# Kernel tuning notes

Hardware: AMD Instinct MI355X
Metric: run time of the kernel (lower is better)

Reference implementation:

```python
import jax, jax.numpy as jnp
import numpy as np
import math

# ---- static config (matches init_kwargs) ----
MUL = 16                       # multiplicity of 0e and 1o irreps in/out
IN_DIM = 4 * MUL               # 16x0e + 16x1o -> 16 + 48 = 64 channels
DIAMETER = 7.0
RADIUS = DIAMETER / 2.0
NRB = 8                        # num_radial_basis
STEPS = (1.0, 1.0, 1.0)
N_PATHS = 5                    # 0x0->0, 1x1->0, 0x1->1, 1x0->1, 1x1->1
WEIGHT_NUMEL = N_PATHS * MUL * MUL  # 1280


def _lattice():
    axes = []
    for st in STEPS:
        s = math.floor(RADIUS / st)
        axes.append(np.arange(-s, s + 1.0) * st)
    return np.stack(np.meshgrid(*axes, indexing='ij'), axis=-1).astype(np.float32)  # [kx,ky,kz,3]


def _radial_emb(r):
    # e3nn soft_one_hot_linspace, basis='smooth_finite', cutoff=True
    values = np.linspace(0.0, RADIUS, NRB + 2)[1:-1].astype(np.float32)
    step = values[1] - values[0]
    diff = (r[..., None] - values) / step
    def u(t):  # soft unit step: exp(-1/t) for t>0 else 0
        return np.where(t > 0.0, np.exp(-1.0 / np.where(t > 0.0, t, 1.0)), 0.0)
    return (1.14136 * math.e ** 2 * u(diff + 1.0) * u(1.0 - diff)).astype(np.float32)


def _spherical_harmonics(lat):
    # normalize=True, normalization='component': Y0 = 1, Y1 = sqrt(3) * unit_vec
    n = np.linalg.norm(lat, axis=-1, keepdims=True)
    unit = np.where(n > 0, lat / np.where(n > 0, n, 1.0), 0.0)
    return np.ones(lat.shape[:-1], np.float32), (math.sqrt(3.0) * unit).astype(np.float32)


_LAT = _lattice()
_EMB = jnp.asarray(_radial_emb(np.linalg.norm(_LAT, axis=-1)))  # [kx,ky,kz,NRB]
_sh0_np, _sh1_np = _spherical_harmonics(_LAT)
_SH0, _SH1 = jnp.asarray(_sh0_np), jnp.asarray(_sh1_np)
_eps_np = np.zeros((3, 3, 3), np.float32)
for _i, _j, _k in [(0, 1, 2), (1, 2, 0), (2, 0, 1)]:
    _eps_np[_i, _j, _k] = 1.0
    _eps_np[_i, _k, _j] = -1.0
_EPS = jnp.asarray(_eps_np)


def _build_kernel(tp_weight):
    """Radial-basis matmul + CG tensor-product -> conv kernel [out,in,kx,ky,kz]."""
    kx, ky, kz = _LAT.shape[:3]
    nk = kx * ky * kz
    w = jnp.einsum('xyzb,bn->xyzn', _EMB, tp_weight) / nk
    w = w.reshape(kx, ky, kz, N_PATHS, MUL, MUL)
    w1, w2, w3, w4, w5 = [w[..., p, :, :] for p in range(N_PATHS)]
    # e3nn path weights ('component' norm, 'element' path norm): sqrt(dim_out / fan_in)
    a0 = math.sqrt(1.0 / (2 * MUL))  # -> 0e: paths 1,2 each mul1*mul2 = MUL
    a1 = math.sqrt(3.0 / (3 * MUL))  # -> 1o: paths 3,4,5
    c1 = a0                          # w3j(0,0,0) = 1
    c2 = a0 / math.sqrt(3.0)         # w3j(1,1,0) = delta/sqrt(3)
    c3 = a1 / math.sqrt(3.0)         # w3j(0,1,1) = delta/sqrt(3)
    c4 = a1 / math.sqrt(3.0)         # w3j(1,0,1) = delta/sqrt(3)
    c5 = a1 / math.sqrt(6.0)         # w3j(1,1,1) = eps/sqrt(6)
    Kss = c1 * _SH0[..., None, None] * w1                                  # [k,u,o]
    Kvs = c2 * jnp.einsum('xyzi,xyzuo->xyzuio', _SH1, w2)                  # [k,u,3,o]
    Ksv = c3 * jnp.einsum('xyzk,xyzuo->xyzuok', _SH1, w3)                  # [k,u,o,3]
    eye3 = jnp.eye(3, dtype=w.dtype)
    Kvv = (c4 * jnp.einsum('xyz,ik,xyzuo->xyzuiok', _SH0, eye3, w4)
           + c5 * jnp.einsum('ijk,xyzj,xyzuo->xyzuiok', _EPS, _SH1, w5))   # [k,u,3,o,3]
    top = jnp.concatenate([Kss, Ksv.reshape(kx, ky, kz, MUL, 3 * MUL)], axis=-1)
    bot = jnp.concatenate([Kvs.reshape(kx, ky, kz, 3 * MUL, MUL),
                           Kvv.reshape(kx, ky, kz, 3 * MUL, 3 * MUL)], axis=-1)
    K = jnp.concatenate([top, bot], axis=-2)                               # [kx,ky,kz,in,out]
    return jnp.transpose(K, (4, 3, 0, 1, 2))                               # oixyz


def setup_inputs() -> dict:
    key = jax.random.key(0)
    k1, k2, k3, k4 = jax.random.split(key, 4)
    x = jax.random.normal(k1, (2, IN_DIM, 40, 40, 40), jnp.float32)
    sc_w0 = jax.random.normal(k2, (MUL, MUL), jnp.float32)
    sc_w1 = jax.random.normal(k3, (MUL, MUL), jnp.float32)
    tp_weight = jax.random.normal(k4, (NRB, WEIGHT_NUMEL), jnp.float32)
    return {"x": x, "sc_w0": sc_w0, "sc_w1": sc_w1, "tp_weight": tp_weight}


def reference(x, sc_w0, sc_w1, tp_weight):
    B = x.shape[0]
    sp = x.shape[2:]
    inv = 1.0 / math.sqrt(MUL)  # e3nn Linear fan-in normalization
    x0 = x[:, :MUL]                                  # [B,MUL,D,H,W]
    x1 = x[:, MUL:].reshape(B, MUL, 3, *sp)          # [B,MUL,3,D,H,W]
    sc0 = jnp.einsum('uo,budhw->bodhw', sc_w0, x0) * inv
    sc1 = jnp.einsum('uo,buidhw->boidhw', sc_w1, x1) * inv
    sc = jnp.concatenate([sc0, sc1.reshape(B, 3 * MUL, *sp)], axis=1)
    K = _build_kernel(tp_weight)
    pad = [(s // 2, s // 2) for s in K.shape[2:]]
    conv = jax.lax.conv_general_dilated(
        x, K, window_strides=(1, 1, 1), padding=pad,
        dimension_numbers=('NCDHW', 'OIDHW', 'NCDHW'))
    return sc + conv
```

## Files before the change

### kernel.cpp

```cpp
#include <hip/hip_runtime.h>
#include <stdint.h>


#define NT_REAL 179
#define NT_PAD  180
#define NPAIR   90

#define XCH  1557376
#define XCHB ((size_t)XCH * 2)

#define HBYTES 35840
#define SEGB   12288
#define NSEG   15
#define NSTEP  120

typedef short s16x8 __attribute__((ext_vector_type(8)));
typedef float f32x4 __attribute__((ext_vector_type(4)));
typedef float f32x16 __attribute__((ext_vector_type(16)));

struct Taps {
  int n;
  short dl16[NT_PAD];
  unsigned char dz[NT_PAD], dy[NT_PAD], dx[NT_PAD];
};
constexpr Taps mk_taps() {
  Taps t{};
  t.n = 0;
  for (int a = 0; a < 7; ++a)
    for (int b = 0; b < 7; ++b)
      for (int c = 0; c < 7; ++c) {
        int d2 = (a-3)*(a-3) + (b-3)*(b-3) + (c-3)*(c-3);
        if (d2 <= 12) {
          t.dz[t.n] = (unsigned char)a; t.dy[t.n] = (unsigned char)b;
          t.dx[t.n] = (unsigned char)c;
          t.dl16[t.n] = (short)((a*14 + b)*16 + c);
          ++t.n;
        }
      }
  for (int i = t.n; i < NT_PAD; ++i) {
    t.dz[i] = 3; t.dy[i] = 3; t.dx[i] = 3; t.dl16[i] = t.dl16[0];
  }
  return t;
}
__device__ constexpr Taps TAPS = mk_taps();
static_assert(mk_taps().n == NT_REAL, "tap count");

struct DL2 { unsigned int v[NPAIR]; };
constexpr DL2 mk_dl2() {
  DL2 d{};
  Taps t = mk_taps();
  for (int p = 0; p < NPAIR; ++p)
    d.v[p] = (unsigned int)(unsigned short)t.dl16[2*p]
           | ((unsigned int)(unsigned short)t.dl16[2*p + 1] << 16);
  return d;
}
__device__ constexpr DL2 DL2V = mk_dl2();

static __device__ inline unsigned short f2bf(float f) {
  unsigned int u = __float_as_uint(f);
  unsigned int r = u + 0x7FFFu + ((u >> 16) & 1u);
  return (unsigned short)(r >> 16);
}

__device__ __forceinline__ void gl_lds16(const void* g, void* s) {
  __builtin_amdgcn_global_load_lds(
      (const __attribute__((address_space(1))) void*)g,
      (__attribute__((address_space(3))) void*)s, 16, 0, 0);
}

__global__ void prep(const float* __restrict__ x, const float* __restrict__ scw0,
                     const float* __restrict__ scw1, const float* __restrict__ tpw,
                     unsigned short* __restrict__ Xp, unsigned short* __restrict__ Bwp) {
  __shared__ float buf[160 * 65];
  int tid = threadIdx.x;

  if (blockIdx.x < 800) {
    int blk = blockIdx.x;
    int ys = blk % 10; int t2 = blk / 10; int iz = t2 % 40; int b = t2 / 40;
    int y0 = ys * 4;
    const float* src = x + (size_t)b * 4096000 + (size_t)iz * 1600 + (size_t)y0 * 40;
    for (int e = tid; e < 64 * 160; e += 256) {
      int ch = e / 160, i = e - ch * 160;
      buf[i * 65 + ch] = src[(size_t)ch * 64000 + i];
    }
    __syncthreads();
    for (int f = tid; f < 160 * 8; f += 256) {
      int i = f >> 3, g = f & 7;
      int yy = i / 40, xx = i - yy * 40;
      s16x8 v;
      #pragma unroll
      for (int j = 0; j < 8; ++j) v[j] = (short)f2bf(buf[i * 65 + g * 8 + j]);
      size_t pos = ((size_t)((b * 46 + iz + 3) * 46 + (y0 + yy + 3)) * 46 + (xx + 3));
      *reinterpret_cast<s16x8*>(Xp + (size_t)g * XCH + pos * 8) = v;
    }
    return;
  }

  int t = blockIdx.x - 800;
  float (*wsm)[16][16] = reinterpret_cast<float (*)[16][16]>(buf);

  int dz = TAPS.dz[t], dy = TAPS.dy[t], dx = TAPS.dx[t];
  float fz = dz - 3.0f, fy = dy - 3.0f, fx = dx - 3.0f;
  float d2 = fz*fz + fy*fy + fx*fx;
  float r = sqrtf(d2);

  const float step = 3.5f / 9.0f;
  const float Cc = 1.14136f * 7.38905609893065f;
  float emb[8];
  for (int bb = 0; bb < 8; ++bb) {
    float diff = (r - step * (bb + 1)) / step;
    float t1 = diff + 1.0f, t2 = 1.0f - diff;
    float u1 = (t1 > 0.0f) ? expf(-1.0f / t1) : 0.0f;
    float u2 = (t2 > 0.0f) ? expf(-1.0f / t2) : 0.0f;
    emb[bb] = Cc * u1 * u2;
  }

  int u = tid >> 4, o = tid & 15;
  for (int p = 0; p < 5; ++p) {
    float acc = 0.0f;
    int nidx = (p * 16 + u) * 16 + o;
    for (int bb = 0; bb < 8; ++bb) acc += emb[bb] * tpw[bb * 1280 + nidx];
    wsm[p][u][o] = acc * (1.0f / 343.0f);
  }
  __syncthreads();

  float invr = (d2 > 0.0f) ? (1.7320508075688772f / r) : 0.0f;
  float sh[3] = { fz * invr, fy * invr, fx * invr };

  bool center = (dz == 3 && dy == 3 && dx == 3);
  bool padt = (t >= NT_REAL);
  const float c1 = 0.17677669529663687f;
  const float c2 = 0.10206207261596575f;
  const float c3 = 0.14433756729740643f;
  const float c4 = 0.14433756729740643f;
  const float c5 = 0.10206207261596575f;
  const float inv = 0.25f;

  for (int e = tid; e < 4096; e += 256) {
    int ich = e & 63, och = e >> 6;
    float v = 0.0f;
    if (!padt) {
      if (och < 16) {
        if (ich < 16) {
          v = c1 * wsm[0][ich][och];
          if (center) v += inv * scw0[ich * 16 + och];
        } else {
          int qq = ich - 16; int uu = qq / 3, ii = qq % 3;
          v = c2 * sh[ii] * wsm[1][uu][och];
        }
      } else {
        int qo = och - 16; int oo = qo / 3, kk = qo % 3;
        if (ich < 16) {
          v = c3 * sh[kk] * wsm[2][ich][oo];
        } else {
          int qi = ich - 16; int uu = qi / 3, ii = qi % 3;
          if (ii == kk) {
            v = c4 * wsm[3][uu][oo];
            if (center) v += inv * scw1[uu * 16 + oo];
          } else {
            int jj = 3 - ii - kk;
            float sgn = (((kk - ii + 3) % 3) == 2) ? 1.0f : -1.0f;
            v = c5 * sgn * sh[jj] * wsm[4][uu][oo];
          }
        }
      }
    }
    int chunk = ich >> 3, j = ich & 7;
    int pair = t >> 1, hi = t & 1;
    int og = och >> 5, col = och & 31;
    size_t idx = ((((size_t)chunk * NPAIR + pair) * 2 + og) * 2 + hi) * 256
               + (size_t)col * 8 + j;
    Bwp[idx] = f2bf(v);
  }
}

__global__ __launch_bounds__(256, 2) void conv3d(
    const unsigned short* __restrict__ Xp,
    const unsigned short* __restrict__ Bwp,
    float* __restrict__ out) {
  __shared__ __align__(16) unsigned char smem[HBYTES + 3 * SEGB];
  unsigned char* BB = smem + HBYTES;

  int blk = blockIdx.x;
  int p = ((blk & 7) << 6) | (blk >> 3);
  if (p >= 500) return;
  int b = p / 250; int rem = p - b * 250;
  int tz = rem / 25, ty = (rem / 5) % 5, tx = rem % 5;

  int tid = threadIdx.x;
  int lane = tid & 63;
  int w = tid >> 6;
  int hi = lane >> 5, r32 = lane & 31;
  int hs = hi << 4;

  size_t hbase = (size_t)(((b * 46 + tz * 4) * 46 + ty * 8) * 46 + tx * 8) * 16;

  int abase = w * 224 + ((r32 >> 3) << 4) + (r32 & 7);

  f32x16 acc[2][2];
  #pragma unroll
  for (int f = 0; f < 2; ++f)
    #pragma unroll
    for (int og = 0; og < 2; ++og)
      #pragma unroll
      for (int e = 0; e < 16; ++e) acc[f][og][e] = 0.0f;

  auto stageB = [&](int st) {
    int cn = st / NSEG, sn = st - cn * NSEG;
    const unsigned char* bg = (const unsigned char*)Bwp
        + ((size_t)cn * NPAIR + sn * 6) * 2048;
    unsigned char* dst = BB + (size_t)(st % 3) * SEGB;
    for (int k = w; k < 12; k += 4)
      gl_lds16(bg + (k << 10) + lane * 16, dst + (k << 10));
  };
  auto stageH = [&](int c) {
    const unsigned char* xc = (const unsigned char*)Xp + (size_t)c * XCHB + hbase;
    for (int k = w; k < 35; k += 4) {
      int sl = (k << 6) + lane;
      int hx = sl & 15; hx = hx > 13 ? 13 : hx;
      int r = sl >> 4;
      int hz = (r * 2341) >> 15;
      int hy = r - hz * 14;
      gl_lds16(xc + ((size_t)((hz * 46 + hy) * 46 + hx)) * 16, smem + (k << 10));
    }
  };

  stageH(0);
  stageB(0); stageB(1);
  asm volatile("s_waitcnt vmcnt(3)" ::: "memory");
  __builtin_amdgcn_s_barrier();

  int t = 0;
  for (int c = 0; c < 8; ++c) {
    if (c > 0) {
      stageH(c);
      stageB(t + 1);
      asm volatile("s_waitcnt vmcnt(3)" ::: "memory");
      __builtin_amdgcn_s_barrier();
    }
    for (int s = 0; s < NSEG; ++s, ++t) {
      if (s < 14 && t + 2 < NSTEP) stageB(t + 2);

      const unsigned char* BSc = BB + (size_t)(t % 3) * SEGB + (size_t)lane * 16;
      s16x8 fa[2][2], fb[2][2];
      {
        unsigned int dlv = DL2V.v[s * 6];
        int dl = (int)((dlv >> hs) & 0xFFFFu);
        const unsigned char* ab = smem + ((size_t)(abase + dl) << 4);
        fa[0][0] = *(const s16x8*)(ab);
        fa[0][1] = *(const s16x8*)(ab + 1024);
        fb[0][0] = *(const s16x8*)(BSc);
        fb[0][1] = *(const s16x8*)(BSc + 1024);
      }
      __builtin_amdgcn_s_setprio(1);
      #pragma unroll
      for (int pp = 0; pp < 6; ++pp) {
        int cur = pp & 1, nxt = cur ^ 1;
        if (pp < 5) {
          unsigned int dlv = DL2V.v[s * 6 + pp + 1];
          int dl = (int)((dlv >> hs) & 0xFFFFu);
          const unsigned char* ab = smem + ((size_t)(abase + dl) << 4);
          fa[nxt][0] = *(const s16x8*)(ab);
          fa[nxt][1] = *(const s16x8*)(ab + 1024);
          const unsigned char* bp = BSc + ((pp + 1) << 11);
          fb[nxt][0] = *(const s16x8*)(bp);
          fb[nxt][1] = *(const s16x8*)(bp + 1024);
        }
        acc[0][0] = __builtin_amdgcn_mfma_f32_32x32x16_bf16(fa[cur][0], fb[cur][0], acc[0][0], 0, 0, 0);
        acc[0][1] = __builtin_amdgcn_mfma_f32_32x32x16_bf16(fa[cur][0], fb[cur][1], acc[0][1], 0, 0, 0);
        acc[1][0] = __builtin_amdgcn_mfma_f32_32x32x16_bf16(fa[cur][1], fb[cur][0], acc[1][0], 0, 0, 0);
        acc[1][1] = __builtin_amdgcn_mfma_f32_32x32x16_bf16(fa[cur][1], fb[cur][1], acc[1][1], 0, 0, 0);
      }
      __builtin_amdgcn_s_setprio(0);

      if (s < 14 && t < NSTEP - 2)
        asm volatile("s_waitcnt vmcnt(3)" ::: "memory");
      else
        asm volatile("s_waitcnt vmcnt(0)" ::: "memory");
      __builtin_amdgcn_s_barrier();
    }
  }

  int col = lane & 31;
  #pragma unroll
  for (int og = 0; og < 2; ++og) {
    #pragma unroll
    for (int f = 0; f < 2; ++f) {
      size_t cb = (size_t)(b * 64 + og * 32 + col) * 64000
                + (size_t)(tz * 4 + w) * 1600
                + (size_t)(tx * 8 + hi * 4);
      #pragma unroll
      for (int ys = 0; ys < 4; ++ys) {
        float* dst = out + cb + (size_t)(ty * 8 + f * 4 + ys) * 40;
        f32x4 v = { acc[f][og][ys * 4 + 0], acc[f][og][ys * 4 + 1],
                    acc[f][og][ys * 4 + 2], acc[f][og][ys * 4 + 3] };
        *reinterpret_cast<f32x4*>(dst) = v;
      }
    }
  }
}

extern "C" void kernel_launch(void* const* d_in, const int* in_sizes, int n_in,
                              void* d_out, int out_size, void* d_ws, size_t ws_size,
                              hipStream_t stream) {
  const float* x    = (const float*)d_in[0];
  const float* scw0 = (const float*)d_in[1];
  const float* scw1 = (const float*)d_in[2];
  const float* tpw  = (const float*)d_in[3];
  float* out = (float*)d_out;

  unsigned short* Xp  = (unsigned short*)d_ws;
  unsigned short* Bwp = Xp + (size_t)8 * XCH;

  hipMemsetAsync(Xp, 0, (size_t)8 * XCH * 2, stream);
  prep<<<800 + NT_PAD, 256, 0, stream>>>(x, scw0, scw1, tpw, Xp, Bwp);
  conv3d<<<512, 256, 0, stream>>>(Xp, Bwp, out);
}
```

Measured before the change: 261.9 us.

## Stream B weights via registers and double-buffer halo tiles in LDS

Weight fragments are no longer staged into a triple-buffered LDS ring. Each wave loads them straight from global memory into registers, double-buffered across 5-pair steps. The input halo now uses two LDS buffers, and the next channel chunk is prefetched one line per step during compute. This removes the per-step barrier, leaving one per chunk, and frees LDS bandwidth, at the cost of many more VGPRs (20 s16x8 of B registers) and redundant global/L2 weight reads per wave.

```diff
diff --git a/kernel.cpp b/kernel.cpp
--- a/kernel.cpp
+++ b/kernel.cpp
@@ -10,9 +10,8 @@
 #define XCHB ((size_t)XCH * 2)
 
 #define HBYTES 35840
-#define SEGB   12288
-#define NSEG   15
-#define NSTEP  120
+#define SEGB   10240
+#define NSEG   18
 
 typedef short s16x8 __attribute__((ext_vector_type(8)));
 typedef float f32x4 __attribute__((ext_vector_type(4)));
@@ -178,8 +177,7 @@
     const unsigned short* __restrict__ Xp,
     const unsigned short* __restrict__ Bwp,
     float* __restrict__ out) {
-  __shared__ __align__(16) unsigned char smem[HBYTES + 3 * SEGB];
-  unsigned char* BB = smem + HBYTES;
+  __shared__ __align__(16) unsigned char smem[2 * HBYTES];
 
   int blk = blockIdx.x;
   int p = ((blk & 7) << 6) | (blk >> 3);
@@ -192,6 +190,7 @@
   int w = tid >> 6;
   int hi = lane >> 5, r32 = lane & 31;
   int hs = hi << 4;
+  size_t ln16 = (size_t)lane * 16;
 
   size_t hbase = (size_t)(((b * 46 + tz * 4) * 46 + ty * 8) * 46 + tx * 8) * 16;
 
@@ -205,81 +204,84 @@
       #pragma unroll
       for (int e = 0; e < 16; ++e) acc[f][og][e] = 0.0f;
 
-  auto stageB = [&](int st) {
-    int cn = st / NSEG, sn = st - cn * NSEG;
-    const unsigned char* bg = (const unsigned char*)Bwp
-        + ((size_t)cn * NPAIR + sn * 6) * 2048;
-    unsigned char* dst = BB + (size_t)(st % 3) * SEGB;
-    for (int k = w; k < 12; k += 4)
-      gl_lds16(bg + (k << 10) + lane * 16, dst + (k << 10));
+  auto stageHLine = [&](int c, int k, unsigned char* dst) {
+    const unsigned char* xc = (const unsigned char*)Xp + (size_t)c * XCHB + hbase;
+    int sl = (k << 6) + lane;
+    int hx = sl & 15; hx = hx > 13 ? 13 : hx;
+    int r = sl >> 4;
+    int hz = (r * 2341) >> 15;
+    int hy = r - hz * 14;
+    gl_lds16(xc + ((size_t)((hz * 46 + hy) * 46 + hx)) * 16, dst + (k << 10));
   };
-  auto stageH = [&](int c) {
-    const unsigned char* xc = (const unsigned char*)Xp + (size_t)c * XCHB + hbase;
-    for (int k = w; k < 35; k += 4) {
-      int sl = (k << 6) + lane;
-      int hx = sl & 15; hx = hx > 13 ? 13 : hx;
-      int r = sl >> 4;
-      int hz = (r * 2341) >> 15;
-      int hy = r - hz * 14;
-      gl_lds16(xc + ((size_t)((hz * 46 + hy) * 46 + hx)) * 16, smem + (k << 10));
-    }
-  };
-
-  stageH(0);
-  stageB(0); stageB(1);
-  asm volatile("s_waitcnt vmcnt(3)" ::: "memory");
+
+  s16x8 bA[5][2], bB[5][2];
+  const unsigned char* bptr = (const unsigned char*)Bwp;
+  const unsigned char* bend = bptr + (size_t)8 * NPAIR * 2048;
+
+  for (int k = w; k < 35; k += 4) stageHLine(0, k, smem);
+  #pragma unroll
+  for (int pp = 0; pp < 5; ++pp) {
+    bA[pp][0] = *(const s16x8*)(bptr + (pp << 11) + ln16);
+    bA[pp][1] = *(const s16x8*)(bptr + (pp << 11) + 1024 + ln16);
+  }
+  bptr += SEGB;
+  asm volatile("s_waitcnt vmcnt(10)" ::: "memory");
   __builtin_amdgcn_s_barrier();
 
-  int t = 0;
+#define CONV_STEP(CUR, NXT, S)                                               \
+  {                                                                          \
+    if (bptr != bend) {                                                      \
+      _Pragma("unroll")                                                      \
+      for (int pp = 0; pp < 5; ++pp) {                                       \
+        NXT[pp][0] = *(const s16x8*)(bptr + (pp << 11) + ln16);              \
+        NXT[pp][1] = *(const s16x8*)(bptr + (pp << 11) + 1024 + ln16);       \
+      }                                                                      \
+      bptr += SEGB;                                                          \
+    }                                                                        \
+    if (c < 7) {                                                             \
+      int L = (S) * 4 + w;                                                   \
+      if (L < 35) stageHLine(c + 1, L, XHn);                                 \
+    }                                                                        \
+    s16x8 fa[2][2];                                                          \
+    {                                                                        \
+      unsigned int dlv = DL2V.v[(S) * 5];                                    \
+      int dl = (int)((dlv >> hs) & 0xFFFFu);                                 \
+      const unsigned char* ab = XH + ((size_t)(abase + dl) << 4);            \
+      fa[0][0] = *(const s16x8*)(ab);                                        \
+      fa[0][1] = *(const s16x8*)(ab + 1024);                                 \
+    }                                                                        \
+    __builtin_amdgcn_s_setprio(1);                                           \
+    _Pragma("unroll")                                                        \
+    for (int pp = 0; pp < 5; ++pp) {                                         \
+      int cur = pp & 1, nxt = cur ^ 1;                                       \
+      if (pp < 4) {                                                          \
+        unsigned int dlv = DL2V.v[(S) * 5 + pp + 1];                         \
+        int dl = (int)((dlv >> hs) & 0xFFFFu);                               \
+        const unsigned char* ab = XH + ((size_t)(abase + dl) << 4);          \
+        fa[nxt][0] = *(const s16x8*)(ab);                                    \
+        fa[nxt][1] = *(const s16x8*)(ab + 1024);                             \
+      }                                                                      \
+      acc[0][0] = __builtin_amdgcn_mfma_f32_32x32x16_bf16(fa[cur][0], CUR[pp][0], acc[0][0], 0, 0, 0); \
+      acc[0][1] = __builtin_amdgcn_mfma_f32_32x32x16_bf16(fa[cur][0], CUR[pp][1], acc[0][1], 0, 0, 0); \
+      acc[1][0] = __builtin_amdgcn_mfma_f32_32x32x16_bf16(fa[cur][1], CUR[pp][0], acc[1][0], 0, 0, 0); \
+      acc[1][1] = __builtin_amdgcn_mfma_f32_32x32x16_bf16(fa[cur][1], CUR[pp][1], acc[1][1], 0, 0, 0); \
+    }                                                                        \
+    __builtin_amdgcn_s_setprio(0);                                           \
+  }
+
   for (int c = 0; c < 8; ++c) {
-    if (c > 0) {
-      stageH(c);
-      stageB(t + 1);
-      asm volatile("s_waitcnt vmcnt(3)" ::: "memory");
+    unsigned char* XH  = smem + (c & 1) * HBYTES;
+    unsigned char* XHn = smem + ((c + 1) & 1) * HBYTES;
+    for (int s2 = 0; s2 < 9; ++s2) {
+      CONV_STEP(bA, bB, (2 * s2));
+      CONV_STEP(bB, bA, (2 * s2 + 1));
+    }
+    if (c < 7) {
+      asm volatile("s_waitcnt vmcnt(10)" ::: "memory");
       __builtin_amdgcn_s_barrier();
     }
-    for (int s = 0; s < NSEG; ++s, ++t) {
-      if (s < 14 && t + 2 < NSTEP) stageB(t + 2);
-
-      const unsigned char* BSc = BB + (size_t)(t % 3) * SEGB + (size_t)lane * 16;
-      s16x8 fa[2][2], fb[2][2];
-      {
-        unsigned int dlv = DL2V.v[s * 6];
-        int dl = (int)((dlv >> hs) & 0xFFFFu);
-        const unsigned char* ab = smem + ((size_t)(abase + dl) << 4);
-        fa[0][0] = *(const s16x8*)(ab);
-        fa[0][1] = *(const s16x8*)(ab + 1024);
-        fb[0][0] = *(const s16x8*)(BSc);
-        fb[0][1] = *(const s16x8*)(BSc + 1024);
-      }
-      __builtin_amdgcn_s_setprio(1);
-      #pragma unroll
-      for (int pp = 0; pp < 6; ++pp) {
-        int cur = pp & 1, nxt = cur ^ 1;
-        if (pp < 5) {
-          unsigned int dlv = DL2V.v[s * 6 + pp + 1];
-          int dl = (int)((dlv >> hs) & 0xFFFFu);
-          const unsigned char* ab = smem + ((size_t)(abase + dl) << 4);
-          fa[nxt][0] = *(const s16x8*)(ab);
-          fa[nxt][1] = *(const s16x8*)(ab + 1024);
-          const unsigned char* bp = BSc + ((pp + 1) << 11);
-          fb[nxt][0] = *(const s16x8*)(bp);
-          fb[nxt][1] = *(const s16x8*)(bp + 1024);
-        }
-        acc[0][0] = __builtin_amdgcn_mfma_f32_32x32x16_bf16(fa[cur][0], fb[cur][0], acc[0][0], 0, 0, 0);
-        acc[0][1] = __builtin_amdgcn_mfma_f32_32x32x16_bf16(fa[cur][0], fb[cur][1], acc[0][1], 0, 0, 0);
-        acc[1][0] = __builtin_amdgcn_mfma_f32_32x32x16_bf16(fa[cur][1], fb[cur][0], acc[1][0], 0, 0, 0);
-        acc[1][1] = __builtin_amdgcn_mfma_f32_32x32x16_bf16(fa[cur][1], fb[cur][1], acc[1][1], 0, 0, 0);
-      }
-      __builtin_amdgcn_s_setprio(0);
-
-      if (s < 14 && t < NSTEP - 2)
-        asm volatile("s_waitcnt vmcnt(3)" ::: "memory");
-      else
-        asm volatile("s_waitcnt vmcnt(0)" ::: "memory");
-      __builtin_amdgcn_s_barrier();
-    }
-  }
+  }
+#undef CONV_STEP
 
   int col = lane & 31;
   #pragma unroll
```

Measured after the change: 264.5 us. About the same (+1.0%).
